# Kernel tuning notes

Measured on AMD Instinct MI355X. Metric: run time of the kernel, lower is better.

## Reference

```python
import jax, jax.numpy as jnp
import numpy as np

N = 100000   # nodes
E = 3200000  # edges (avg degree 32)
D = 128      # in_channels
H = 128      # hidden_channels
A, S, ETH = 3, 2, 3  # head output dims


def _w(k, o, i):
    return jax.random.normal(k, (o, i), dtype=jnp.float32) / np.sqrt(i).astype(np.float32)


def setup_inputs() -> dict:
    key = jax.random.key(0)
    ks = jax.random.split(key, 20)
    x = jax.random.normal(ks[0], (N, D), dtype=jnp.float32)
    edge_index = jax.random.randint(ks[1], (2, E), 0, N, dtype=jnp.int64)
    inp = {"x": x, "edge_index": edge_index}
    # SAGEConv params: Wl applied to mean-aggregated neighbors, Wr to root, plus bias
    dims = [("1", D, H), ("2", H, H), ("3", H, H), ("a", H, A), ("s", H, S), ("e", H, ETH)]
    ki = 2
    for tag, i, o in dims:
        inp[f"W{tag}l"] = _w(ks[ki], o, i); ki += 1
        inp[f"W{tag}r"] = _w(ks[ki], o, i); ki += 1
        inp[f"b{tag}"] = jnp.zeros((o,), dtype=jnp.float32)
    return inp


def _sage(x, src, dst, inv_deg, Wl, Wr, b):
    # mean aggregation of source features onto destination nodes, then linear
    agg = jax.ops.segment_sum(x[src], dst, num_segments=N) * inv_deg  # [N, d]
    return agg @ Wl.T + x @ Wr.T + b


def reference(x, edge_index,
              W1l, W1r, b1, W2l, W2r, b2, W3l, W3r, b3,
              Wal, War, ba, Wsl, Wsr, bs, Wel, Wer, be):
    src, dst = edge_index[0], edge_index[1]
    deg = jax.ops.segment_sum(jnp.ones((E,), jnp.float32), dst, num_segments=N)
    inv_deg = (1.0 / jnp.maximum(deg, 1.0))[:, None]  # [N,1]
    h = jax.nn.relu(_sage(x, src, dst, inv_deg, W1l, W1r, b1))
    h = jax.nn.relu(_sage(h, src, dst, inv_deg, W2l, W2r, b2))
    h = jax.nn.relu(_sage(h, src, dst, inv_deg, W3l, W3r, b3))
    age_out = _sage(h, src, dst, inv_deg, Wal, War, ba)
    sex_out = _sage(h, src, dst, inv_deg, Wsl, Wsr, bs)
    eth_out = _sage(h, src, dst, inv_deg, Wel, Wer, be)
    return (age_out, sex_out, eth_out)
```

## Files before the change

kernel.cpp:

```cpp
#include <hip/hip_runtime.h>

#define TPB 256
#define NB1 256
#define NBUCK 512

using half4_t = __attribute__((ext_vector_type(4))) _Float16;
using half8_t = __attribute__((ext_vector_type(8))) _Float16;
using f32x4 = __attribute__((ext_vector_type(4))) float;


__global__ __launch_bounds__(256) void hist1_k(const int* __restrict__ ei,
                                               int* __restrict__ hist, int E, int stripe) {
  __shared__ int h[NBUCK];
  for (int i = threadIdx.x; i < NBUCK; i += 256) h[i] = 0;
  __syncthreads();
  int b0 = blockIdx.x * stripe;
  int b1 = min(b0 + stripe, E);
  for (int e = b0 + threadIdx.x; e < b1; e += 256) atomicAdd(&h[ei[E + e] >> 8], 1);
  __syncthreads();
  for (int i = threadIdx.x; i < NBUCK; i += 256) hist[i * NB1 + blockIdx.x] = h[i];
}

__global__ void scan1_k(const int* __restrict__ src, int* __restrict__ out,
                        int* __restrict__ chunk, int n) {
  __shared__ int sh[TPB];
  int i = blockIdx.x * TPB + threadIdx.x;
  int v = (i < n) ? src[i] : 0;
  sh[threadIdx.x] = v;
  __syncthreads();
  for (int off = 1; off < TPB; off <<= 1) {
    int t = (threadIdx.x >= off) ? sh[threadIdx.x - off] : 0;
    __syncthreads();
    sh[threadIdx.x] += t;
    __syncthreads();
  }
  if (i < n) out[i] = sh[threadIdx.x] - v;
  if (threadIdx.x == TPB - 1) chunk[blockIdx.x] = sh[TPB - 1];
}

__global__ void scan2_k(int* __restrict__ chunk, int nb) {
  __shared__ int sh[512];
  int v = (threadIdx.x < nb) ? chunk[threadIdx.x] : 0;
  sh[threadIdx.x] = v;
  __syncthreads();
  for (int off = 1; off < 512; off <<= 1) {
    int t = (threadIdx.x >= off) ? sh[threadIdx.x - off] : 0;
    __syncthreads();
    sh[threadIdx.x] += t;
    __syncthreads();
  }
  if (threadIdx.x < nb) chunk[threadIdx.x] = sh[threadIdx.x] - v;
}

__global__ void scan3_k(int* __restrict__ out, const int* __restrict__ chunk, int n) {
  int i = blockIdx.x * TPB + threadIdx.x;
  if (i < n) out[i] += chunk[blockIdx.x];
}

__global__ __launch_bounds__(256) void scatter1_k(const int* __restrict__ ei,
                                                  const int* __restrict__ base,
                                                  unsigned* __restrict__ ebuf, int E,
                                                  int stripe) {
  __shared__ int cur[NBUCK];
  for (int i = threadIdx.x; i < NBUCK; i += 256) cur[i] = base[i * NB1 + blockIdx.x];
  __syncthreads();
  int b0 = blockIdx.x * stripe;
  int b1 = min(b0 + stripe, E);
  for (int e = b0 + threadIdx.x; e < b1; e += 256) {
    int s = ei[e];
    int d = ei[E + e];
    int p = atomicAdd(&cur[d >> 8], 1);
    ebuf[p] = (unsigned)s | ((unsigned)(d & 255) << 24);
  }
}

__global__ __launch_bounds__(256) void build_k(const unsigned* __restrict__ ebuf,
                                               const int* __restrict__ base,
                                               int* __restrict__ row_start,
                                               int* __restrict__ deg,
                                               float* __restrict__ invd,
                                               int* __restrict__ csr, int N, int E) {
  __shared__ int h[256];
  __shared__ int excl[256];
  __shared__ int bse[2];
  int b = blockIdx.x;
  int t = threadIdx.x;
  if (t == 0) {
    bse[0] = base[b * NB1];
    bse[1] = (b + 1 < NBUCK) ? base[(b + 1) * NB1] : E;
  }
  h[t] = 0;
  __syncthreads();
  int bs = bse[0], be = bse[1];
  for (int e = bs + t; e < be; e += 256) atomicAdd(&h[ebuf[e] >> 24], 1);
  __syncthreads();
  int v = h[t];
  excl[t] = v;
  __syncthreads();
  for (int off = 1; off < 256; off <<= 1) {
    int tv = (t >= off) ? excl[t - off] : 0;
    __syncthreads();
    excl[t] += tv;
    __syncthreads();
  }
  int ex = excl[t] - v;
  int node = b * 256 + t;
  if (node < N) {
    row_start[node] = bs + ex;
    deg[node] = v;
    invd[node] = 1.0f / fmaxf((float)v, 1.0f);
  }
  h[t] = bs + ex;
  __syncthreads();
  for (int e = bs + t; e < be; e += 256) {
    unsigned p = ebuf[e];
    int pos = atomicAdd(&h[p >> 24], 1);
    csr[pos] = (int)(p & 0xFFFFFFu);
  }
}


__global__ void prep_k(const float* __restrict__ x, _Float16* __restrict__ xh, int n4,
                       const float* __restrict__ w0, const float* __restrict__ w1,
                       const float* __restrict__ w2, const float* __restrict__ w3,
                       const float* __restrict__ w4, const float* __restrict__ w5,
                       _Float16* __restrict__ wh,
                       const float* __restrict__ Wal, const float* __restrict__ War,
                       const float* __restrict__ ba, const float* __restrict__ Wsl,
                       const float* __restrict__ Wsr, const float* __restrict__ bsx,
                       const float* __restrict__ Wel, const float* __restrict__ Wer,
                       const float* __restrict__ be, _Float16* __restrict__ Wcat,
                       float* __restrict__ bcat) {
  int t = blockIdx.x * TPB + threadIdx.x;
  if (t < n4) {
    float4 v = ((const float4*)x)[t];
    half4_t o;
    o.x = (_Float16)v.x; o.y = (_Float16)v.y; o.z = (_Float16)v.z; o.w = (_Float16)v.w;
    ((half4_t*)xh)[t] = o;
  }
  if (t < 6 * 4096) {
    int which = t >> 12, i = t & 4095;
    const float* src = which == 0 ? w0 : which == 1 ? w1 : which == 2 ? w2
                     : which == 3 ? w3 : which == 4 ? w4 : w5;
    float4 v = ((const float4*)src)[i];
    half4_t o;
    o.x = (_Float16)v.x; o.y = (_Float16)v.y; o.z = (_Float16)v.z; o.w = (_Float16)v.w;
    ((half4_t*)wh)[(size_t)which * 4096 + i] = o;
  }
  if (t < 2048) {
    float v = 0.f;
    if (t < 384) v = Wal[t];
    else if (t < 640) v = Wsl[t - 384];
    else if (t < 1024) v = Wel[t - 640];
    else if (t < 1408) v = War[t - 1024];
    else if (t < 1664) v = Wsr[t - 1408];
    else v = Wer[t - 1664];
    Wcat[t] = (_Float16)v;
  }
  if (t < 16) {
    float b = 0.f;
    if (t >= 8 && t < 11) b = ba[t - 8];
    else if (t >= 11 && t < 13) b = bsx[t - 11];
    else if (t >= 13) b = be[t - 13];
    bcat[t] = b;
  }
}


__global__ __launch_bounds__(256) void agg128_k(const _Float16* __restrict__ hb,
                                                const int* __restrict__ csr,
                                                const int* __restrict__ row_start,
                                                const int* __restrict__ deg,
                                                const float* __restrict__ invd,
                                                _Float16* __restrict__ out, int n) {
  int node = (blockIdx.x << 2) + (threadIdx.x >> 6);
  if (node >= n) return;
  int lane = threadIdx.x & 63;
  int g = lane >> 4;
  int l = lane & 15;
  int s = row_start[node];
  int c = deg[node];
  const _Float16* base = hb + (l << 3);
  float a0 = 0.f, a1 = 0.f, a2 = 0.f, a3 = 0.f;
  float a4 = 0.f, a5 = 0.f, a6 = 0.f, a7 = 0.f;
  int j = 0;
  if (c >= 16) {
    int id[4];
#pragma unroll
    for (int p = 0; p < 4; ++p) id[p] = csr[s + 4 * p + g];
    while (true) {
      half8_t v[4];
#pragma unroll
      for (int p = 0; p < 4; ++p) v[p] = *(const half8_t*)&base[(size_t)id[p] * 128];
      j += 16;
      bool more = (j + 16 <= c);
      if (more) {
#pragma unroll
        for (int p = 0; p < 4; ++p) id[p] = csr[s + j + 4 * p + g];
      }
#pragma unroll
      for (int p = 0; p < 4; ++p) {
        a0 += (float)v[p][0]; a1 += (float)v[p][1];
        a2 += (float)v[p][2]; a3 += (float)v[p][3];
        a4 += (float)v[p][4]; a5 += (float)v[p][5];
        a6 += (float)v[p][6]; a7 += (float)v[p][7];
      }
      if (!more) break;
    }
  }
  if (j < c) {
    int cm1 = c - 1;
#pragma unroll
    for (int p = 0; p < 4; ++p) {
      int e = j + 4 * p + g;
      float m = (e < c) ? 1.f : 0.f;
      int id = csr[s + min(e, cm1)];
      half8_t v = *(const half8_t*)&base[(size_t)id * 128];
      a0 = fmaf(m, (float)v[0], a0); a1 = fmaf(m, (float)v[1], a1);
      a2 = fmaf(m, (float)v[2], a2); a3 = fmaf(m, (float)v[3], a3);
      a4 = fmaf(m, (float)v[4], a4); a5 = fmaf(m, (float)v[5], a5);
      a6 = fmaf(m, (float)v[6], a6); a7 = fmaf(m, (float)v[7], a7);
    }
  }
  a0 += __shfl_xor(a0, 16); a1 += __shfl_xor(a1, 16);
  a2 += __shfl_xor(a2, 16); a3 += __shfl_xor(a3, 16);
  a4 += __shfl_xor(a4, 16); a5 += __shfl_xor(a5, 16);
  a6 += __shfl_xor(a6, 16); a7 += __shfl_xor(a7, 16);
  a0 += __shfl_xor(a0, 32); a1 += __shfl_xor(a1, 32);
  a2 += __shfl_xor(a2, 32); a3 += __shfl_xor(a3, 32);
  a4 += __shfl_xor(a4, 32); a5 += __shfl_xor(a5, 32);
  a6 += __shfl_xor(a6, 32); a7 += __shfl_xor(a7, 32);
  if (g == 0) {
    float w = invd[node];
    half8_t r;
    r[0] = (_Float16)(a0 * w); r[1] = (_Float16)(a1 * w);
    r[2] = (_Float16)(a2 * w); r[3] = (_Float16)(a3 * w);
    r[4] = (_Float16)(a4 * w); r[5] = (_Float16)(a5 * w);
    r[6] = (_Float16)(a6 * w); r[7] = (_Float16)(a7 * w);
    *(half8_t*)&out[(size_t)node * 128 + (l << 3)] = r;
  }
}


__global__ __launch_bounds__(256) void gemm2_k(
    const _Float16* __restrict__ Aagg, const _Float16* __restrict__ Ah,
    const _Float16* __restrict__ Wh,
    const float* __restrict__ bias, _Float16* __restrict__ outh, int n) {
  __shared__ _Float16 Ws[32768];
  int tid = threadIdx.x;
  int wave = tid >> 6;
  int lane = tid & 63;
  int g = lane >> 4;
  int l = lane & 15;
  int m0 = blockIdx.x * 64 + wave * 16;
  int arow = m0 + l;
  bool valid = arow < n;

  half8_t afA[4], afH[4];
  size_t abase = (size_t)arow * 128 + g * 8;
  if (valid) {
#pragma unroll
    for (int kb = 0; kb < 4; ++kb) afA[kb] = *(const half8_t*)&Aagg[abase + kb * 32];
#pragma unroll
    for (int kb = 0; kb < 4; ++kb) afH[kb] = *(const half8_t*)&Ah[abase + kb * 32];
  } else {
#pragma unroll
    for (int kb = 0; kb < 4; ++kb) {
#pragma unroll
      for (int jj = 0; jj < 8; ++jj) { afA[kb][jj] = (_Float16)0; afH[kb][jj] = (_Float16)0; }
    }
  }

#pragma unroll
  for (int it = 0; it < 16; ++it) {
    int ci = tid + it * 256;
    int row = ci >> 4;
    int kc = ci & 15;
    float4 v = *(const float4*)&Wh[(size_t)row * 128 + kc * 8];
    *(float4*)&Ws[(size_t)row * 128 + ((kc ^ (row & 7)) * 8)] = v;
  }
  __syncthreads();

  f32x4 acc[8];
#pragma unroll
  for (int ct = 0; ct < 8; ++ct) acc[ct] = (f32x4){0.f, 0.f, 0.f, 0.f};

#pragma unroll
  for (int kb = 0; kb < 4; ++kb) {
#pragma unroll
    for (int ct = 0; ct < 8; ++ct) {
      int row = ct * 16 + l;
      half8_t bf = *(const half8_t*)&Ws[(size_t)row * 128 + (((kb * 4 + g) ^ (l & 7)) * 8)];
      acc[ct] = __builtin_amdgcn_mfma_f32_16x16x32_f16(afA[kb], bf, acc[ct], 0, 0, 0);
    }
  }
#pragma unroll
  for (int kb = 0; kb < 4; ++kb) {
#pragma unroll
    for (int ct = 0; ct < 8; ++ct) {
      int row = 128 + ct * 16 + l;
      half8_t bf = *(const half8_t*)&Ws[(size_t)row * 128 + (((kb * 4 + g) ^ (l & 7)) * 8)];
      acc[ct] = __builtin_amdgcn_mfma_f32_16x16x32_f16(afH[kb], bf, acc[ct], 0, 0, 0);
    }
  }

#pragma unroll
  for (int ct = 0; ct < 8; ++ct) {
    int col = ct * 16 + l;
    float bc = bias[col];
#pragma unroll
    for (int r = 0; r < 4; ++r) {
      int row = m0 + g * 4 + r;
      if (row < n) {
        float v = fmaxf(acc[ct][r] + bc, 0.f);
        outh[(size_t)row * 128 + col] = (_Float16)v;
      }
    }
  }
}


__global__ __launch_bounds__(256) void head_gemm_k(const _Float16* __restrict__ h,
                                                   const _Float16* __restrict__ Wcat,
                                                   const float* __restrict__ bcat,
                                                   float* __restrict__ head_g,
                                                   float* __restrict__ head_r, int n) {
  __shared__ _Float16 Ws[2048];
  __shared__ float bs[16];
  int tid = threadIdx.x;
  {
    int row = tid >> 4, kc = tid & 15;
    float4 v = *(const float4*)&Wcat[(size_t)row * 128 + kc * 8];
    *(float4*)&Ws[(size_t)row * 128 + ((kc ^ (row & 7)) * 8)] = v;
    if (tid < 16) bs[tid] = bcat[tid];
  }
  __syncthreads();
  int wave = tid >> 6;
  int lane = tid & 63;
  int g = lane >> 4;
  int l = lane & 15;
  int m0 = blockIdx.x * 64 + wave * 16;
  int arow = m0 + l;
  bool valid = arow < n;
  size_t abase = (size_t)arow * 128 + g * 8;
  f32x4 acc = (f32x4){0.f, 0.f, 0.f, 0.f};
#pragma unroll
  for (int kb = 0; kb < 4; ++kb) {
    half8_t af;
    if (valid) {
      af = *(const half8_t*)&h[abase + kb * 32];
    } else {
#pragma unroll
      for (int jj = 0; jj < 8; ++jj) af[jj] = (_Float16)0;
    }
    half8_t bf = *(const half8_t*)&Ws[(size_t)l * 128 + (((kb * 4 + g) ^ (l & 7)) * 8)];
    acc = __builtin_amdgcn_mfma_f32_16x16x32_f16(af, bf, acc, 0, 0, 0);
  }
  float bc = bs[l];
#pragma unroll
  for (int r = 0; r < 4; ++r) {
    int row = m0 + g * 4 + r;
    if (row < n) {
      float v = acc[r] + bc;
      if (l < 8) head_g[(size_t)row * 8 + l] = v;
      else head_r[(size_t)row * 8 + (l - 8)] = v;
    }
  }
}


__global__ void agg8_k(const float* __restrict__ head_g, const float* __restrict__ head_r,
                       const int* __restrict__ csr, const int* __restrict__ row_start,
                       const int* __restrict__ deg, const float* __restrict__ invd,
                       float* __restrict__ out, int n) {
  int node = (blockIdx.x << 2) + (threadIdx.x >> 6);
  if (node >= n) return;
  int lane = threadIdx.x & 63;
  int c2 = lane & 3;
  int g = lane >> 2;
  int s = row_start[node], cnt = deg[node];
  float ax = 0.f, ay = 0.f;
  int j = 0;
  for (; j + 32 <= cnt; j += 32) {
#pragma unroll
    for (int p = 0; p < 2; ++p) {
      int id = csr[s + j + 16 * p + g];
      float2 v = *(const float2*)&head_g[(size_t)id * 8 + 2 * c2];
      ax += v.x;
      ay += v.y;
    }
  }
  if (j < cnt) {
    int cm1 = cnt - 1;
#pragma unroll
    for (int p = 0; p < 2; ++p) {
      int e = j + 16 * p + g;
      float m = (e < cnt) ? 1.f : 0.f;
      int id = csr[s + min(e, cm1)];
      float2 v = *(const float2*)&head_g[(size_t)id * 8 + 2 * c2];
      ax = fmaf(m, v.x, ax);
      ay = fmaf(m, v.y, ay);
    }
  }
  ax += __shfl_xor(ax, 4);  ay += __shfl_xor(ay, 4);
  ax += __shfl_xor(ax, 8);  ay += __shfl_xor(ay, 8);
  ax += __shfl_xor(ax, 16); ay += __shfl_xor(ay, 16);
  ax += __shfl_xor(ax, 32); ay += __shfl_xor(ay, 32);
  if (g == 0) {
    float w = invd[node];
    float r0 = ax * w + head_r[(size_t)node * 8 + 2 * c2];
    float r1 = ay * w + head_r[(size_t)node * 8 + 2 * c2 + 1];
    float rr[2] = {r0, r1};
#pragma unroll
    for (int q = 0; q < 2; ++q) {
      int f = 2 * c2 + q;
      float r = rr[q];
      if (f < 3) out[(size_t)node * 3 + f] = r;
      else if (f < 5) out[(size_t)3 * n + (size_t)node * 2 + (f - 3)] = r;
      else out[(size_t)5 * n + (size_t)node * 3 + (f - 5)] = r;
    }
  }
}


extern "C" void kernel_launch(void* const* d_in, const int* in_sizes, int n_in,
                              void* d_out, int out_size, void* d_ws, size_t ws_size,
                              hipStream_t stream) {
  const float* x = (const float*)d_in[0];
  const int* ei = (const int*)d_in[1];
  const float* W1l = (const float*)d_in[2];
  const float* W1r = (const float*)d_in[3];
  const float* b1 = (const float*)d_in[4];
  const float* W2l = (const float*)d_in[5];
  const float* W2r = (const float*)d_in[6];
  const float* b2 = (const float*)d_in[7];
  const float* W3l = (const float*)d_in[8];
  const float* W3r = (const float*)d_in[9];
  const float* b3 = (const float*)d_in[10];
  const float* Wal = (const float*)d_in[11];
  const float* War = (const float*)d_in[12];
  const float* ba = (const float*)d_in[13];
  const float* Wsl = (const float*)d_in[14];
  const float* Wsr = (const float*)d_in[15];
  const float* bsx = (const float*)d_in[16];
  const float* Wel = (const float*)d_in[17];
  const float* Wer = (const float*)d_in[18];
  const float* be = (const float*)d_in[19];

  int N = in_sizes[0] / 128;
  int E = in_sizes[1] / 2;
  int NBKT = (N + 255) >> 8;

  char* w = (char*)d_ws;
  auto alloc = [&](size_t b) {
    char* p = w;
    w += (b + 255) & ~(size_t)255;
    return p;
  };
  int* deg = (int*)alloc((size_t)N * 4);
  int* row_start = (int*)alloc((size_t)N * 4);
  float* invd = (float*)alloc((size_t)N * 4);
  int* hist = (int*)alloc((size_t)NBUCK * NB1 * 4);
  int* chunk = (int*)alloc(512 * 4);
  int* csr = (int*)alloc((size_t)E * 4);
  size_t xh_bytes = (size_t)N * 128 * 2;
  size_t ebuf_bytes = (size_t)E * 4;
  char* region = (char*)alloc(xh_bytes > ebuf_bytes ? xh_bytes : ebuf_bytes);
  unsigned* ebuf = (unsigned*)region;
  _Float16* xh = (_Float16*)region;
  _Float16* aggh = (_Float16*)alloc((size_t)N * 128 * 2);
  _Float16* hA = (_Float16*)alloc((size_t)N * 128 * 2);
  _Float16* hB = (_Float16*)alloc((size_t)N * 128 * 2);
  _Float16* wh = (_Float16*)alloc((size_t)6 * 16384 * 2);
  _Float16* Wcat = (_Float16*)alloc(2048 * 2);
  float* bcat = (float*)alloc(16 * 4);
  float* head_g = (float*)alloc((size_t)N * 8 * 4);
  float* head_r = (float*)alloc((size_t)N * 8 * 4);

  int stripe = (((E + NB1 - 1) / NB1) + 255) & ~255;
  int nscan = NBUCK * NB1;
  int nbScan = (nscan + TPB - 1) / TPB;
  int nbNode = (N + 3) / 4;
  int nbM = (N + 63) / 64;
  int nbC = (N * 32 + TPB - 1) / TPB;

  hist1_k<<<NB1, 256, 0, stream>>>(ei, hist, E, stripe);
  scan1_k<<<nbScan, TPB, 0, stream>>>(hist, hist, chunk, nscan);
  scan2_k<<<1, 512, 0, stream>>>(chunk, nbScan);
  scan3_k<<<nbScan, TPB, 0, stream>>>(hist, chunk, nscan);
  scatter1_k<<<NB1, 256, 0, stream>>>(ei, hist, ebuf, E, stripe);
  build_k<<<NBKT, 256, 0, stream>>>(ebuf, hist, row_start, deg, invd, csr, N, E);

  prep_k<<<nbC, TPB, 0, stream>>>(x, xh, N * 32, W1l, W1r, W2l, W2r, W3l, W3r, wh,
                                  Wal, War, ba, Wsl, Wsr, bsx, Wel, Wer, be, Wcat, bcat);

  agg128_k<<<nbNode, TPB, 0, stream>>>(xh, csr, row_start, deg, invd, aggh, N);
  gemm2_k<<<nbM, TPB, 0, stream>>>(aggh, xh, wh + 0 * 16384, b1, hA, N);
  agg128_k<<<nbNode, TPB, 0, stream>>>(hA, csr, row_start, deg, invd, aggh, N);
  gemm2_k<<<nbM, TPB, 0, stream>>>(aggh, hA, wh + 2 * 16384, b2, hB, N);
  agg128_k<<<nbNode, TPB, 0, stream>>>(hB, csr, row_start, deg, invd, aggh, N);
  gemm2_k<<<nbM, TPB, 0, stream>>>(aggh, hB, wh + 4 * 16384, b3, hA, N);
  head_gemm_k<<<nbM, TPB, 0, stream>>>(hA, Wcat, bcat, head_g, head_r, N);
  agg8_k<<<nbNode, TPB, 0, stream>>>(head_g, head_r, csr, row_start, deg, invd,
                                     (float*)d_out, N);
}
```

Measured before the change: 681.4 us.

## Split node features into four 32-channel planes and aggregate per plane

Feature tensors are stored as four planar 32-channel slabs instead of row-major 128 channels. Aggregation runs once per plane, so each gather touches a smaller working set (6.4 MB per plane) that is more likely to stay in cache. The aggregation also sums in fp16 vectors instead of fp32 scalars. That adds precision risk and four times as many aggregation launches and CSR index reads, and the GEMMs now read and write through plane-strided addresses.

Result: slower. 846.1 us (+24.2%).

```diff
diff --git a/kernel.cpp b/kernel.cpp
--- a/kernel.cpp
+++ b/kernel.cpp
@@ -120,7 +120,8 @@
 }
 
 
-__global__ void prep_k(const float* __restrict__ x, _Float16* __restrict__ xh, int n4,
+__global__ void prep_k(const float* __restrict__ x, _Float16* __restrict__ xhp, int n4,
+                       int N,
                        const float* __restrict__ w0, const float* __restrict__ w1,
                        const float* __restrict__ w2, const float* __restrict__ w3,
                        const float* __restrict__ w4, const float* __restrict__ w5,
@@ -136,7 +137,9 @@
     float4 v = ((const float4*)x)[t];
     half4_t o;
     o.x = (_Float16)v.x; o.y = (_Float16)v.y; o.z = (_Float16)v.z; o.w = (_Float16)v.w;
-    ((half4_t*)xh)[t] = o;
+    int node = t >> 5, w = t & 31;
+    int plane = w >> 3, off = (w & 7) * 4;
+    *(half4_t*)&xhp[(size_t)plane * N * 32 + (size_t)node * 32 + off] = o;
   }
   if (t < 6 * 4096) {
     int which = t >> 12, i = t & 4095;
@@ -167,77 +170,73 @@
 }
 
 
-__global__ __launch_bounds__(256) void agg128_k(const _Float16* __restrict__ hb,
-                                                const int* __restrict__ csr,
-                                                const int* __restrict__ row_start,
-                                                const int* __restrict__ deg,
-                                                const float* __restrict__ invd,
-                                                _Float16* __restrict__ out, int n) {
+static __device__ inline half8_t h8_shfl_xor(half8_t v, int m) {
+  union U { half8_t h; int i[4]; } u, r;
+  u.h = v;
+#pragma unroll
+  for (int k = 0; k < 4; ++k) r.i[k] = __shfl_xor(u.i[k], m);
+  return r.h;
+}
+
+__global__ __launch_bounds__(256) void agg32_k(const _Float16* __restrict__ hp,
+                                               const int* __restrict__ csr,
+                                               const int* __restrict__ row_start,
+                                               const int* __restrict__ deg,
+                                               const float* __restrict__ invd,
+                                               _Float16* __restrict__ outp, int n) {
   int node = (blockIdx.x << 2) + (threadIdx.x >> 6);
   if (node >= n) return;
   int lane = threadIdx.x & 63;
-  int g = lane >> 4;
-  int l = lane & 15;
+  int slot = lane >> 2;
+  int q = lane & 3;
   int s = row_start[node];
   int c = deg[node];
-  const _Float16* base = hb + (l << 3);
-  float a0 = 0.f, a1 = 0.f, a2 = 0.f, a3 = 0.f;
-  float a4 = 0.f, a5 = 0.f, a6 = 0.f, a7 = 0.f;
+  const _Float16* base = hp + (q << 3);
+  half8_t acc;
+#pragma unroll
+  for (int k = 0; k < 8; ++k) acc[k] = (_Float16)0;
   int j = 0;
-  if (c >= 16) {
-    int id[4];
-#pragma unroll
-    for (int p = 0; p < 4; ++p) id[p] = csr[s + 4 * p + g];
+  if (c >= 32) {
+    int idA = csr[s + slot];
+    int idB = csr[s + 16 + slot];
     while (true) {
-      half8_t v[4];
-#pragma unroll
-      for (int p = 0; p < 4; ++p) v[p] = *(const half8_t*)&base[(size_t)id[p] * 128];
-      j += 16;
-      bool more = (j + 16 <= c);
+      half8_t vA = *(const half8_t*)&base[(size_t)idA * 32];
+      half8_t vB = *(const half8_t*)&base[(size_t)idB * 32];
+      j += 32;
+      bool more = (j + 32 <= c);
       if (more) {
-#pragma unroll
-        for (int p = 0; p < 4; ++p) id[p] = csr[s + j + 4 * p + g];
+        idA = csr[s + j + slot];
+        idB = csr[s + j + 16 + slot];
       }
-#pragma unroll
-      for (int p = 0; p < 4; ++p) {
-        a0 += (float)v[p][0]; a1 += (float)v[p][1];
-        a2 += (float)v[p][2]; a3 += (float)v[p][3];
-        a4 += (float)v[p][4]; a5 += (float)v[p][5];
-        a6 += (float)v[p][6]; a7 += (float)v[p][7];
-      }
+      acc += vA;
+      acc += vB;
       if (!more) break;
     }
   }
   if (j < c) {
     int cm1 = c - 1;
 #pragma unroll
-    for (int p = 0; p < 4; ++p) {
-      int e = j + 4 * p + g;
-      float m = (e < c) ? 1.f : 0.f;
+    for (int p = 0; p < 2; ++p) {
+      int e = j + p * 16 + slot;
+      _Float16 m = (e < c) ? (_Float16)1 : (_Float16)0;
       int id = csr[s + min(e, cm1)];
-      half8_t v = *(const half8_t*)&base[(size_t)id * 128];
-      a0 = fmaf(m, (float)v[0], a0); a1 = fmaf(m, (float)v[1], a1);
-      a2 = fmaf(m, (float)v[2], a2); a3 = fmaf(m, (float)v[3], a3);
-      a4 = fmaf(m, (float)v[4], a4); a5 = fmaf(m, (float)v[5], a5);
-      a6 = fmaf(m, (float)v[6], a6); a7 = fmaf(m, (float)v[7], a7);
-    }
-  }
-  a0 += __shfl_xor(a0, 16); a1 += __shfl_xor(a1, 16);
-  a2 += __shfl_xor(a2, 16); a3 += __shfl_xor(a3, 16);
-  a4 += __shfl_xor(a4, 16); a5 += __shfl_xor(a5, 16);
-  a6 += __shfl_xor(a6, 16); a7 += __shfl_xor(a7, 16);
-  a0 += __shfl_xor(a0, 32); a1 += __shfl_xor(a1, 32);
-  a2 += __shfl_xor(a2, 32); a3 += __shfl_xor(a3, 32);
-  a4 += __shfl_xor(a4, 32); a5 += __shfl_xor(a5, 32);
-  a6 += __shfl_xor(a6, 32); a7 += __shfl_xor(a7, 32);
-  if (g == 0) {
+      half8_t v = *(const half8_t*)&base[(size_t)id * 32];
+      half8_t mm;
+#pragma unroll
+      for (int k = 0; k < 8; ++k) mm[k] = m;
+      acc += v * mm;
+    }
+  }
+  acc += h8_shfl_xor(acc, 4);
+  acc += h8_shfl_xor(acc, 8);
+  acc += h8_shfl_xor(acc, 16);
+  acc += h8_shfl_xor(acc, 32);
+  if (slot == 0) {
     float w = invd[node];
     half8_t r;
-    r[0] = (_Float16)(a0 * w); r[1] = (_Float16)(a1 * w);
-    r[2] = (_Float16)(a2 * w); r[3] = (_Float16)(a3 * w);
-    r[4] = (_Float16)(a4 * w); r[5] = (_Float16)(a5 * w);
-    r[6] = (_Float16)(a6 * w); r[7] = (_Float16)(a7 * w);
-    *(half8_t*)&out[(size_t)node * 128 + (l << 3)] = r;
+#pragma unroll
+    for (int k = 0; k < 8; ++k) r[k] = (_Float16)((float)acc[k] * w);
+    *(half8_t*)&outp[(size_t)node * 32 + (q << 3)] = r;
   }
 }
 
@@ -245,7 +244,7 @@
 __global__ __launch_bounds__(256) void gemm2_k(
     const _Float16* __restrict__ Aagg, const _Float16* __restrict__ Ah,
     const _Float16* __restrict__ Wh,
-    const float* __restrict__ bias, _Float16* __restrict__ outh, int n) {
+    const float* __restrict__ bias, _Float16* __restrict__ outh, int n, int N) {
   __shared__ _Float16 Ws[32768];
   int tid = threadIdx.x;
   int wave = tid >> 6;
@@ -255,14 +254,16 @@
   int m0 = blockIdx.x * 64 + wave * 16;
   int arow = m0 + l;
   bool valid = arow < n;
+  size_t pstride = (size_t)N * 32;
 
   half8_t afA[4], afH[4];
-  size_t abase = (size_t)arow * 128 + g * 8;
   if (valid) {
 #pragma unroll
-    for (int kb = 0; kb < 4; ++kb) afA[kb] = *(const half8_t*)&Aagg[abase + kb * 32];
-#pragma unroll
-    for (int kb = 0; kb < 4; ++kb) afH[kb] = *(const half8_t*)&Ah[abase + kb * 32];
+    for (int kb = 0; kb < 4; ++kb)
+      afA[kb] = *(const half8_t*)&Aagg[(size_t)kb * pstride + (size_t)arow * 32 + g * 8];
+#pragma unroll
+    for (int kb = 0; kb < 4; ++kb)
+      afH[kb] = *(const half8_t*)&Ah[(size_t)kb * pstride + (size_t)arow * 32 + g * 8];
   } else {
 #pragma unroll
     for (int kb = 0; kb < 4; ++kb) {
@@ -308,12 +309,13 @@
   for (int ct = 0; ct < 8; ++ct) {
     int col = ct * 16 + l;
     float bc = bias[col];
+    size_t pbase = (size_t)(ct >> 1) * pstride + (size_t)((ct & 1) * 16 + l);
 #pragma unroll
     for (int r = 0; r < 4; ++r) {
       int row = m0 + g * 4 + r;
       if (row < n) {
         float v = fmaxf(acc[ct][r] + bc, 0.f);
-        outh[(size_t)row * 128 + col] = (_Float16)v;
+        outh[pbase + (size_t)row * 32] = (_Float16)v;
       }
     }
   }
@@ -324,7 +326,8 @@
                                                    const _Float16* __restrict__ Wcat,
                                                    const float* __restrict__ bcat,
                                                    float* __restrict__ head_g,
-                                                   float* __restrict__ head_r, int n) {
+                                                   float* __restrict__ head_r, int n,
+                                                   int N) {
   __shared__ _Float16 Ws[2048];
   __shared__ float bs[16];
   int tid = threadIdx.x;
@@ -342,13 +345,13 @@
   int m0 = blockIdx.x * 64 + wave * 16;
   int arow = m0 + l;
   bool valid = arow < n;
-  size_t abase = (size_t)arow * 128 + g * 8;
+  size_t pstride = (size_t)N * 32;
   f32x4 acc = (f32x4){0.f, 0.f, 0.f, 0.f};
 #pragma unroll
   for (int kb = 0; kb < 4; ++kb) {
     half8_t af;
     if (valid) {
-      af = *(const half8_t*)&h[abase + kb * 32];
+      af = *(const half8_t*)&h[(size_t)kb * pstride + (size_t)arow * 32 + g * 8];
     } else {
 #pragma unroll
       for (int jj = 0; jj < 8; ++jj) af[jj] = (_Float16)0;
@@ -483,6 +486,7 @@
   int nbNode = (N + 3) / 4;
   int nbM = (N + 63) / 64;
   int nbC = (N * 32 + TPB - 1) / TPB;
+  size_t pstride = (size_t)N * 32;
 
   hist1_k<<<NB1, 256, 0, stream>>>(ei, hist, E, stripe);
   scan1_k<<<nbScan, TPB, 0, stream>>>(hist, hist, chunk, nscan);
@@ -491,16 +495,22 @@
   scatter1_k<<<NB1, 256, 0, stream>>>(ei, hist, ebuf, E, stripe);
   build_k<<<NBKT, 256, 0, stream>>>(ebuf, hist, row_start, deg, invd, csr, N, E);
 
-  prep_k<<<nbC, TPB, 0, stream>>>(x, xh, N * 32, W1l, W1r, W2l, W2r, W3l, W3r, wh,
+  prep_k<<<nbC, TPB, 0, stream>>>(x, xh, N * 32, N, W1l, W1r, W2l, W2r, W3l, W3r, wh,
                                   Wal, War, ba, Wsl, Wsr, bsx, Wel, Wer, be, Wcat, bcat);
 
-  agg128_k<<<nbNode, TPB, 0, stream>>>(xh, csr, row_start, deg, invd, aggh, N);
-  gemm2_k<<<nbM, TPB, 0, stream>>>(aggh, xh, wh + 0 * 16384, b1, hA, N);
-  agg128_k<<<nbNode, TPB, 0, stream>>>(hA, csr, row_start, deg, invd, aggh, N);
-  gemm2_k<<<nbM, TPB, 0, stream>>>(aggh, hA, wh + 2 * 16384, b2, hB, N);
-  agg128_k<<<nbNode, TPB, 0, stream>>>(hB, csr, row_start, deg, invd, aggh, N);
-  gemm2_k<<<nbM, TPB, 0, stream>>>(aggh, hB, wh + 4 * 16384, b3, hA, N);
-  head_gemm_k<<<nbM, TPB, 0, stream>>>(hA, Wcat, bcat, head_g, head_r, N);
+  for (int p = 0; p < 4; ++p)
+    agg32_k<<<nbNode, TPB, 0, stream>>>(xh + p * pstride, csr, row_start, deg, invd,
+                                        aggh + p * pstride, N);
+  gemm2_k<<<nbM, TPB, 0, stream>>>(aggh, xh, wh + 0 * 16384, b1, hA, N, N);
+  for (int p = 0; p < 4; ++p)
+    agg32_k<<<nbNode, TPB, 0, stream>>>(hA + p * pstride, csr, row_start, deg, invd,
+                                        aggh + p * pstride, N);
+  gemm2_k<<<nbM, TPB, 0, stream>>>(aggh, hA, wh + 2 * 16384, b2, hB, N, N);
+  for (int p = 0; p < 4; ++p)
+    agg32_k<<<nbNode, TPB, 0, stream>>>(hB + p * pstride, csr, row_start, deg, invd,
+                                        aggh + p * pstride, N);
+  gemm2_k<<<nbM, TPB, 0, stream>>>(aggh, hB, wh + 4 * 16384, b3, hA, N, N);
+  head_gemm_k<<<nbM, TPB, 0, stream>>>(hA, Wcat, bcat, head_g, head_r, N, N);
   agg8_k<<<nbNode, TPB, 0, stream>>>(head_g, head_r, csr, row_start, deg, invd,
                                      (float*)d_out, N);
 }
```

## Replace two-level bucketed CSR build with global-atomic degree count and fill

Applied to the files above, without the earlier changes.

Replaces the two-pass bucket sort (shared-memory histogram, scatter into bucketed buffer, per-bucket local sort) with a direct CSR build: global atomic degree count, scan over nodes, then a fill pass using global atomic cursors per destination. This removes the intermediate ebuf pass and the large histogram scan, but relies on millions of global atomics to random addresses and makes the neighbor order within each row nondeterministic. That order change can hurt gather locality in the aggregation kernels. Degree zeroing is folded into the prep kernel.

Result: slower. 972.4 us (+42.7%).

```diff
diff --git a/kernel.cpp b/kernel.cpp
--- a/kernel.cpp
+++ b/kernel.cpp
@@ -1,24 +1,15 @@
 #include <hip/hip_runtime.h>
 
 #define TPB 256
-#define NB1 256
-#define NBUCK 512
 
 using half4_t = __attribute__((ext_vector_type(4))) _Float16;
 using half8_t = __attribute__((ext_vector_type(8))) _Float16;
 using f32x4 = __attribute__((ext_vector_type(4))) float;
 
 
-__global__ __launch_bounds__(256) void hist1_k(const int* __restrict__ ei,
-                                               int* __restrict__ hist, int E, int stripe) {
-  __shared__ int h[NBUCK];
-  for (int i = threadIdx.x; i < NBUCK; i += 256) h[i] = 0;
-  __syncthreads();
-  int b0 = blockIdx.x * stripe;
-  int b1 = min(b0 + stripe, E);
-  for (int e = b0 + threadIdx.x; e < b1; e += 256) atomicAdd(&h[ei[E + e] >> 8], 1);
-  __syncthreads();
-  for (int i = threadIdx.x; i < NBUCK; i += 256) hist[i * NB1 + blockIdx.x] = h[i];
+__global__ void deg_k(const int* __restrict__ ei, int* __restrict__ deg, int E) {
+  int e = blockIdx.x * TPB + threadIdx.x;
+  if (e < E) atomicAdd(&deg[ei[E + e]], 1);
 }
 
 __global__ void scan1_k(const int* __restrict__ src, int* __restrict__ out,
@@ -52,75 +43,32 @@
   if (threadIdx.x < nb) chunk[threadIdx.x] = sh[threadIdx.x] - v;
 }
 
-__global__ void scan3_k(int* __restrict__ out, const int* __restrict__ chunk, int n) {
+__global__ void scan3b_k(int* __restrict__ row_start, const int* __restrict__ chunk,
+                         int* __restrict__ cursor, const int* __restrict__ deg,
+                         float* __restrict__ invd, int n) {
   int i = blockIdx.x * TPB + threadIdx.x;
-  if (i < n) out[i] += chunk[blockIdx.x];
-}
-
-__global__ __launch_bounds__(256) void scatter1_k(const int* __restrict__ ei,
-                                                  const int* __restrict__ base,
-                                                  unsigned* __restrict__ ebuf, int E,
-                                                  int stripe) {
-  __shared__ int cur[NBUCK];
-  for (int i = threadIdx.x; i < NBUCK; i += 256) cur[i] = base[i * NB1 + blockIdx.x];
-  __syncthreads();
-  int b0 = blockIdx.x * stripe;
-  int b1 = min(b0 + stripe, E);
-  for (int e = b0 + threadIdx.x; e < b1; e += 256) {
+  if (i < n) {
+    int rs = row_start[i] + chunk[blockIdx.x];
+    row_start[i] = rs;
+    cursor[i] = rs;
+    invd[i] = 1.0f / fmaxf((float)deg[i], 1.0f);
+  }
+}
+
+__global__ void fill_k(const int* __restrict__ ei, int* __restrict__ cursor,
+                       int* __restrict__ csr, int E) {
+  int e = blockIdx.x * TPB + threadIdx.x;
+  if (e < E) {
     int s = ei[e];
     int d = ei[E + e];
-    int p = atomicAdd(&cur[d >> 8], 1);
-    ebuf[p] = (unsigned)s | ((unsigned)(d & 255) << 24);
-  }
-}
-
-__global__ __launch_bounds__(256) void build_k(const unsigned* __restrict__ ebuf,
-                                               const int* __restrict__ base,
-                                               int* __restrict__ row_start,
-                                               int* __restrict__ deg,
-                                               float* __restrict__ invd,
-                                               int* __restrict__ csr, int N, int E) {
-  __shared__ int h[256];
-  __shared__ int excl[256];
-  __shared__ int bse[2];
-  int b = blockIdx.x;
-  int t = threadIdx.x;
-  if (t == 0) {
-    bse[0] = base[b * NB1];
-    bse[1] = (b + 1 < NBUCK) ? base[(b + 1) * NB1] : E;
-  }
-  h[t] = 0;
-  __syncthreads();
-  int bs = bse[0], be = bse[1];
-  for (int e = bs + t; e < be; e += 256) atomicAdd(&h[ebuf[e] >> 24], 1);
-  __syncthreads();
-  int v = h[t];
-  excl[t] = v;
-  __syncthreads();
-  for (int off = 1; off < 256; off <<= 1) {
-    int tv = (t >= off) ? excl[t - off] : 0;
-    __syncthreads();
-    excl[t] += tv;
-    __syncthreads();
-  }
-  int ex = excl[t] - v;
-  int node = b * 256 + t;
-  if (node < N) {
-    row_start[node] = bs + ex;
-    deg[node] = v;
-    invd[node] = 1.0f / fmaxf((float)v, 1.0f);
-  }
-  h[t] = bs + ex;
-  __syncthreads();
-  for (int e = bs + t; e < be; e += 256) {
-    unsigned p = ebuf[e];
-    int pos = atomicAdd(&h[p >> 24], 1);
-    csr[pos] = (int)(p & 0xFFFFFFu);
+    int pos = atomicAdd(&cursor[d], 1);
+    csr[pos] = s;
   }
 }
 
 
 __global__ void prep_k(const float* __restrict__ x, _Float16* __restrict__ xh, int n4,
+                       int* __restrict__ deg, int N,
                        const float* __restrict__ w0, const float* __restrict__ w1,
                        const float* __restrict__ w2, const float* __restrict__ w3,
                        const float* __restrict__ w4, const float* __restrict__ w5,
@@ -138,6 +86,7 @@
     o.x = (_Float16)v.x; o.y = (_Float16)v.y; o.z = (_Float16)v.z; o.w = (_Float16)v.w;
     ((half4_t*)xh)[t] = o;
   }
+  if (t < N) deg[t] = 0;
   if (t < 6 * 4096) {
     int which = t >> 12, i = t & 4095;
     const float* src = which == 0 ? w0 : which == 1 ? w1 : which == 2 ? w2
@@ -449,7 +398,6 @@
 
   int N = in_sizes[0] / 128;
   int E = in_sizes[1] / 2;
-  int NBKT = (N + 255) >> 8;
 
   char* w = (char*)d_ws;
   auto alloc = [&](size_t b) {
@@ -459,15 +407,11 @@
   };
   int* deg = (int*)alloc((size_t)N * 4);
   int* row_start = (int*)alloc((size_t)N * 4);
+  int* cursor = (int*)alloc((size_t)N * 4);
   float* invd = (float*)alloc((size_t)N * 4);
-  int* hist = (int*)alloc((size_t)NBUCK * NB1 * 4);
   int* chunk = (int*)alloc(512 * 4);
   int* csr = (int*)alloc((size_t)E * 4);
-  size_t xh_bytes = (size_t)N * 128 * 2;
-  size_t ebuf_bytes = (size_t)E * 4;
-  char* region = (char*)alloc(xh_bytes > ebuf_bytes ? xh_bytes : ebuf_bytes);
-  unsigned* ebuf = (unsigned*)region;
-  _Float16* xh = (_Float16*)region;
+  _Float16* xh = (_Float16*)alloc((size_t)N * 128 * 2);
   _Float16* aggh = (_Float16*)alloc((size_t)N * 128 * 2);
   _Float16* hA = (_Float16*)alloc((size_t)N * 128 * 2);
   _Float16* hB = (_Float16*)alloc((size_t)N * 128 * 2);
@@ -477,22 +421,20 @@
   float* head_g = (float*)alloc((size_t)N * 8 * 4);
   float* head_r = (float*)alloc((size_t)N * 8 * 4);
 
-  int stripe = (((E + NB1 - 1) / NB1) + 255) & ~255;
-  int nscan = NBUCK * NB1;
-  int nbScan = (nscan + TPB - 1) / TPB;
   int nbNode = (N + 3) / 4;
   int nbM = (N + 63) / 64;
   int nbC = (N * 32 + TPB - 1) / TPB;
-
-  hist1_k<<<NB1, 256, 0, stream>>>(ei, hist, E, stripe);
-  scan1_k<<<nbScan, TPB, 0, stream>>>(hist, hist, chunk, nscan);
+  int nbE = (E + TPB - 1) / TPB;
+  int nbScan = (N + TPB - 1) / TPB;
+
+  prep_k<<<nbC, TPB, 0, stream>>>(x, xh, N * 32, deg, N, W1l, W1r, W2l, W2r, W3l, W3r,
+                                  wh, Wal, War, ba, Wsl, Wsr, bsx, Wel, Wer, be, Wcat,
+                                  bcat);
+  deg_k<<<nbE, TPB, 0, stream>>>(ei, deg, E);
+  scan1_k<<<nbScan, TPB, 0, stream>>>(deg, row_start, chunk, N);
   scan2_k<<<1, 512, 0, stream>>>(chunk, nbScan);
-  scan3_k<<<nbScan, TPB, 0, stream>>>(hist, chunk, nscan);
-  scatter1_k<<<NB1, 256, 0, stream>>>(ei, hist, ebuf, E, stripe);
-  build_k<<<NBKT, 256, 0, stream>>>(ebuf, hist, row_start, deg, invd, csr, N, E);
-
-  prep_k<<<nbC, TPB, 0, stream>>>(x, xh, N * 32, W1l, W1r, W2l, W2r, W3l, W3r, wh,
-                                  Wal, War, ba, Wsl, Wsr, bsx, Wel, Wer, be, Wcat, bcat);
+  scan3b_k<<<nbScan, TPB, 0, stream>>>(row_start, chunk, cursor, deg, invd, N);
+  fill_k<<<nbE, TPB, 0, stream>>>(ei, cursor, csr, E);
 
   agg128_k<<<nbNode, TPB, 0, stream>>>(xh, csr, row_start, deg, invd, aggh, N);
   gemm2_k<<<nbM, TPB, 0, stream>>>(aggh, xh, wh + 0 * 16384, b1, hA, N);
```

## Fuse histogram with prep, fold scan fixup into consumers, fuse head GEMM

Applied to the files above, without the earlier changes.

Merges the edge histogram and the input/weight fp16 conversion into one launch, which needs separate ebuf and xh buffers instead of an aliased region. Drops the scan3 pass by adding the per-chunk offsets directly in scatter and build. Fuses the head projection into the last layer GEMM epilogue: the ReLU output goes to shared memory and is multiplied by the concatenated head weights, so the layer-3 hidden state is never written to or reread from global memory. This saves launches and a full N×128 round trip, at the cost of extra workspace and a heavier GEMM epilogue.

Measured after the change: 656.2 us. 3.7% less time.

```diff
diff --git a/kernel.cpp b/kernel.cpp
--- a/kernel.cpp
+++ b/kernel.cpp
@@ -9,16 +9,64 @@
 using f32x4 = __attribute__((ext_vector_type(4))) float;
 
 
-__global__ __launch_bounds__(256) void hist1_k(const int* __restrict__ ei,
-                                               int* __restrict__ hist, int E, int stripe) {
+__global__ __launch_bounds__(256) void histprep_k(
+    const int* __restrict__ ei, int* __restrict__ hist, int E, int stripe,
+    const float* __restrict__ x, _Float16* __restrict__ xh, int n4,
+    const float* __restrict__ w0, const float* __restrict__ w1,
+    const float* __restrict__ w2, const float* __restrict__ w3,
+    const float* __restrict__ w4, const float* __restrict__ w5,
+    _Float16* __restrict__ wh,
+    const float* __restrict__ Wal, const float* __restrict__ War,
+    const float* __restrict__ ba, const float* __restrict__ Wsl,
+    const float* __restrict__ Wsr, const float* __restrict__ bsx,
+    const float* __restrict__ Wel, const float* __restrict__ Wer,
+    const float* __restrict__ be, _Float16* __restrict__ Wcat,
+    float* __restrict__ bcat) {
   __shared__ int h[NBUCK];
-  for (int i = threadIdx.x; i < NBUCK; i += 256) h[i] = 0;
-  __syncthreads();
-  int b0 = blockIdx.x * stripe;
-  int b1 = min(b0 + stripe, E);
-  for (int e = b0 + threadIdx.x; e < b1; e += 256) atomicAdd(&h[ei[E + e] >> 8], 1);
-  __syncthreads();
-  for (int i = threadIdx.x; i < NBUCK; i += 256) hist[i * NB1 + blockIdx.x] = h[i];
+  int b = blockIdx.x;
+  if (b < NB1) {
+    for (int i = threadIdx.x; i < NBUCK; i += 256) h[i] = 0;
+    __syncthreads();
+    int b0 = b * stripe;
+    int b1 = min(b0 + stripe, E);
+    for (int e = b0 + threadIdx.x; e < b1; e += 256) atomicAdd(&h[ei[E + e] >> 8], 1);
+    __syncthreads();
+    for (int i = threadIdx.x; i < NBUCK; i += 256) hist[i * NB1 + b] = h[i];
+    return;
+  }
+  int t = (b - NB1) * TPB + threadIdx.x;
+  if (t < n4) {
+    float4 v = ((const float4*)x)[t];
+    half4_t o;
+    o.x = (_Float16)v.x; o.y = (_Float16)v.y; o.z = (_Float16)v.z; o.w = (_Float16)v.w;
+    ((half4_t*)xh)[t] = o;
+  }
+  if (t < 6 * 4096) {
+    int which = t >> 12, i = t & 4095;
+    const float* src = which == 0 ? w0 : which == 1 ? w1 : which == 2 ? w2
+                     : which == 3 ? w3 : which == 4 ? w4 : w5;
+    float4 v = ((const float4*)src)[i];
+    half4_t o;
+    o.x = (_Float16)v.x; o.y = (_Float16)v.y; o.z = (_Float16)v.z; o.w = (_Float16)v.w;
+    ((half4_t*)wh)[(size_t)which * 4096 + i] = o;
+  }
+  if (t < 2048) {
+    float v = 0.f;
+    if (t < 384) v = Wal[t];
+    else if (t < 640) v = Wsl[t - 384];
+    else if (t < 1024) v = Wel[t - 640];
+    else if (t < 1408) v = War[t - 1024];
+    else if (t < 1664) v = Wsr[t - 1408];
+    else v = Wer[t - 1664];
+    Wcat[t] = (_Float16)v;
+  }
+  if (t < 16) {
+    float bb = 0.f;
+    if (t >= 8 && t < 11) bb = ba[t - 8];
+    else if (t >= 11 && t < 13) bb = bsx[t - 11];
+    else if (t >= 13) bb = be[t - 13];
+    bcat[t] = bb;
+  }
 }
 
 __global__ void scan1_k(const int* __restrict__ src, int* __restrict__ out,
@@ -52,17 +100,15 @@
   if (threadIdx.x < nb) chunk[threadIdx.x] = sh[threadIdx.x] - v;
 }
 
-__global__ void scan3_k(int* __restrict__ out, const int* __restrict__ chunk, int n) {
-  int i = blockIdx.x * TPB + threadIdx.x;
-  if (i < n) out[i] += chunk[blockIdx.x];
-}
 
 __global__ __launch_bounds__(256) void scatter1_k(const int* __restrict__ ei,
                                                   const int* __restrict__ base,
+                                                  const int* __restrict__ chunk,
                                                   unsigned* __restrict__ ebuf, int E,
                                                   int stripe) {
   __shared__ int cur[NBUCK];
-  for (int i = threadIdx.x; i < NBUCK; i += 256) cur[i] = base[i * NB1 + blockIdx.x];
+  for (int i = threadIdx.x; i < NBUCK; i += 256)
+    cur[i] = base[i * NB1 + blockIdx.x] + chunk[i];
   __syncthreads();
   int b0 = blockIdx.x * stripe;
   int b1 = min(b0 + stripe, E);
@@ -76,6 +122,7 @@
 
 __global__ __launch_bounds__(256) void build_k(const unsigned* __restrict__ ebuf,
                                                const int* __restrict__ base,
+                                               const int* __restrict__ chunk,
                                                int* __restrict__ row_start,
                                                int* __restrict__ deg,
                                                float* __restrict__ invd,
@@ -86,8 +133,8 @@
   int b = blockIdx.x;
   int t = threadIdx.x;
   if (t == 0) {
-    bse[0] = base[b * NB1];
-    bse[1] = (b + 1 < NBUCK) ? base[(b + 1) * NB1] : E;
+    bse[0] = base[b * NB1] + chunk[b];
+    bse[1] = (b + 1 < NBUCK) ? base[(b + 1) * NB1] + chunk[b + 1] : E;
   }
   h[t] = 0;
   __syncthreads();
@@ -116,53 +163,6 @@
     unsigned p = ebuf[e];
     int pos = atomicAdd(&h[p >> 24], 1);
     csr[pos] = (int)(p & 0xFFFFFFu);
-  }
-}
-
-
-__global__ void prep_k(const float* __restrict__ x, _Float16* __restrict__ xh, int n4,
-                       const float* __restrict__ w0, const float* __restrict__ w1,
-                       const float* __restrict__ w2, const float* __restrict__ w3,
-                       const float* __restrict__ w4, const float* __restrict__ w5,
-                       _Float16* __restrict__ wh,
-                       const float* __restrict__ Wal, const float* __restrict__ War,
-                       const float* __restrict__ ba, const float* __restrict__ Wsl,
-                       const float* __restrict__ Wsr, const float* __restrict__ bsx,
-                       const float* __restrict__ Wel, const float* __restrict__ Wer,
-                       const float* __restrict__ be, _Float16* __restrict__ Wcat,
-                       float* __restrict__ bcat) {
-  int t = blockIdx.x * TPB + threadIdx.x;
-  if (t < n4) {
-    float4 v = ((const float4*)x)[t];
-    half4_t o;
-    o.x = (_Float16)v.x; o.y = (_Float16)v.y; o.z = (_Float16)v.z; o.w = (_Float16)v.w;
-    ((half4_t*)xh)[t] = o;
-  }
-  if (t < 6 * 4096) {
-    int which = t >> 12, i = t & 4095;
-    const float* src = which == 0 ? w0 : which == 1 ? w1 : which == 2 ? w2
-                     : which == 3 ? w3 : which == 4 ? w4 : w5;
-    float4 v = ((const float4*)src)[i];
-    half4_t o;
-    o.x = (_Float16)v.x; o.y = (_Float16)v.y; o.z = (_Float16)v.z; o.w = (_Float16)v.w;
-    ((half4_t*)wh)[(size_t)which * 4096 + i] = o;
-  }
-  if (t < 2048) {
-    float v = 0.f;
-    if (t < 384) v = Wal[t];
-    else if (t < 640) v = Wsl[t - 384];
-    else if (t < 1024) v = Wel[t - 640];
-    else if (t < 1408) v = War[t - 1024];
-    else if (t < 1664) v = Wsr[t - 1408];
-    else v = Wer[t - 1664];
-    Wcat[t] = (_Float16)v;
-  }
-  if (t < 16) {
-    float b = 0.f;
-    if (t >= 8 && t < 11) b = ba[t - 8];
-    else if (t >= 11 && t < 13) b = bsx[t - 11];
-    else if (t >= 13) b = be[t - 13];
-    bcat[t] = b;
   }
 }
 
@@ -245,7 +245,9 @@
 __global__ __launch_bounds__(256) void gemm2_k(
     const _Float16* __restrict__ Aagg, const _Float16* __restrict__ Ah,
     const _Float16* __restrict__ Wh,
-    const float* __restrict__ bias, _Float16* __restrict__ outh, int n) {
+    const float* __restrict__ bias, _Float16* __restrict__ outh,
+    const _Float16* __restrict__ Wcat, const float* __restrict__ bcat,
+    float* __restrict__ head_g, float* __restrict__ head_r, int n, int mode) {
   __shared__ _Float16 Ws[32768];
   int tid = threadIdx.x;
   int wave = tid >> 6;
@@ -304,66 +306,48 @@
     }
   }
 
-#pragma unroll
-  for (int ct = 0; ct < 8; ++ct) {
-    int col = ct * 16 + l;
-    float bc = bias[col];
+  if (mode == 0) {
+#pragma unroll
+    for (int ct = 0; ct < 8; ++ct) {
+      int col = ct * 16 + l;
+      float bc = bias[col];
+#pragma unroll
+      for (int r = 0; r < 4; ++r) {
+        int row = m0 + g * 4 + r;
+        if (row < n) {
+          float v = fmaxf(acc[ct][r] + bc, 0.f);
+          outh[(size_t)row * 128 + col] = (_Float16)v;
+        }
+      }
+    }
+  } else {
+    __syncthreads();
+    _Float16* Hs = Ws + wave * 2048;
+#pragma unroll
+    for (int ct = 0; ct < 8; ++ct) {
+      int col = ct * 16 + l;
+      float bc = bias[col];
+#pragma unroll
+      for (int r = 0; r < 4; ++r) {
+        Hs[(g * 4 + r) * 128 + col] = (_Float16)fmaxf(acc[ct][r] + bc, 0.f);
+      }
+    }
+    f32x4 ah = (f32x4){0.f, 0.f, 0.f, 0.f};
+#pragma unroll
+    for (int kb = 0; kb < 4; ++kb) {
+      half8_t af = *(const half8_t*)&Hs[l * 128 + kb * 32 + g * 8];
+      half8_t bf = *(const half8_t*)&Wcat[(size_t)l * 128 + kb * 32 + g * 8];
+      ah = __builtin_amdgcn_mfma_f32_16x16x32_f16(af, bf, ah, 0, 0, 0);
+    }
+    float bc = bcat[l];
 #pragma unroll
     for (int r = 0; r < 4; ++r) {
       int row = m0 + g * 4 + r;
       if (row < n) {
-        float v = fmaxf(acc[ct][r] + bc, 0.f);
-        outh[(size_t)row * 128 + col] = (_Float16)v;
+        float v = ah[r] + bc;
+        if (l < 8) head_g[(size_t)row * 8 + l] = v;
+        else head_r[(size_t)row * 8 + (l - 8)] = v;
       }
-    }
-  }
-}
-
-
-__global__ __launch_bounds__(256) void head_gemm_k(const _Float16* __restrict__ h,
-                                                   const _Float16* __restrict__ Wcat,
-                                                   const float* __restrict__ bcat,
-                                                   float* __restrict__ head_g,
-                                                   float* __restrict__ head_r, int n) {
-  __shared__ _Float16 Ws[2048];
-  __shared__ float bs[16];
-  int tid = threadIdx.x;
-  {
-    int row = tid >> 4, kc = tid & 15;
-    float4 v = *(const float4*)&Wcat[(size_t)row * 128 + kc * 8];
-    *(float4*)&Ws[(size_t)row * 128 + ((kc ^ (row & 7)) * 8)] = v;
-    if (tid < 16) bs[tid] = bcat[tid];
-  }
-  __syncthreads();
-  int wave = tid >> 6;
-  int lane = tid & 63;
-  int g = lane >> 4;
-  int l = lane & 15;
-  int m0 = blockIdx.x * 64 + wave * 16;
-  int arow = m0 + l;
-  bool valid = arow < n;
-  size_t abase = (size_t)arow * 128 + g * 8;
-  f32x4 acc = (f32x4){0.f, 0.f, 0.f, 0.f};
-#pragma unroll
-  for (int kb = 0; kb < 4; ++kb) {
-    half8_t af;
-    if (valid) {
-      af = *(const half8_t*)&h[abase + kb * 32];
-    } else {
-#pragma unroll
-      for (int jj = 0; jj < 8; ++jj) af[jj] = (_Float16)0;
-    }
-    half8_t bf = *(const half8_t*)&Ws[(size_t)l * 128 + (((kb * 4 + g) ^ (l & 7)) * 8)];
-    acc = __builtin_amdgcn_mfma_f32_16x16x32_f16(af, bf, acc, 0, 0, 0);
-  }
-  float bc = bs[l];
-#pragma unroll
-  for (int r = 0; r < 4; ++r) {
-    int row = m0 + g * 4 + r;
-    if (row < n) {
-      float v = acc[r] + bc;
-      if (l < 8) head_g[(size_t)row * 8 + l] = v;
-      else head_r[(size_t)row * 8 + (l - 8)] = v;
     }
   }
 }
@@ -463,11 +447,8 @@
   int* hist = (int*)alloc((size_t)NBUCK * NB1 * 4);
   int* chunk = (int*)alloc(512 * 4);
   int* csr = (int*)alloc((size_t)E * 4);
-  size_t xh_bytes = (size_t)N * 128 * 2;
-  size_t ebuf_bytes = (size_t)E * 4;
-  char* region = (char*)alloc(xh_bytes > ebuf_bytes ? xh_bytes : ebuf_bytes);
-  unsigned* ebuf = (unsigned*)region;
-  _Float16* xh = (_Float16*)region;
+  unsigned* ebuf = (unsigned*)alloc((size_t)E * 4);
+  _Float16* xh = (_Float16*)alloc((size_t)N * 128 * 2);
   _Float16* aggh = (_Float16*)alloc((size_t)N * 128 * 2);
   _Float16* hA = (_Float16*)alloc((size_t)N * 128 * 2);
   _Float16* hB = (_Float16*)alloc((size_t)N * 128 * 2);
@@ -484,23 +465,24 @@
   int nbM = (N + 63) / 64;
   int nbC = (N * 32 + TPB - 1) / TPB;
 
-  hist1_k<<<NB1, 256, 0, stream>>>(ei, hist, E, stripe);
+  histprep_k<<<NB1 + nbC, TPB, 0, stream>>>(ei, hist, E, stripe, x, xh, N * 32,
+                                            W1l, W1r, W2l, W2r, W3l, W3r, wh,
+                                            Wal, War, ba, Wsl, Wsr, bsx, Wel, Wer,
+                                            be, Wcat, bcat);
   scan1_k<<<nbScan, TPB, 0, stream>>>(hist, hist, chunk, nscan);
   scan2_k<<<1, 512, 0, stream>>>(chunk, nbScan);
-  scan3_k<<<nbScan, TPB, 0, stream>>>(hist, chunk, nscan);
-  scatter1_k<<<NB1, 256, 0, stream>>>(ei, hist, ebuf, E, stripe);
-  build_k<<<NBKT, 256, 0, stream>>>(ebuf, hist, row_start, deg, invd, csr, N, E);
-
-  prep_k<<<nbC, TPB, 0, stream>>>(x, xh, N * 32, W1l, W1r, W2l, W2r, W3l, W3r, wh,
-                                  Wal, War, ba, Wsl, Wsr, bsx, Wel, Wer, be, Wcat, bcat);
+  scatter1_k<<<NB1, 256, 0, stream>>>(ei, hist, chunk, ebuf, E, stripe);
+  build_k<<<NBKT, 256, 0, stream>>>(ebuf, hist, chunk, row_start, deg, invd, csr, N, E);
 
   agg128_k<<<nbNode, TPB, 0, stream>>>(xh, csr, row_start, deg, invd, aggh, N);
-  gemm2_k<<<nbM, TPB, 0, stream>>>(aggh, xh, wh + 0 * 16384, b1, hA, N);
+  gemm2_k<<<nbM, TPB, 0, stream>>>(aggh, xh, wh + 0 * 16384, b1, hA, nullptr, nullptr,
+                                   nullptr, nullptr, N, 0);
   agg128_k<<<nbNode, TPB, 0, stream>>>(hA, csr, row_start, deg, invd, aggh, N);
-  gemm2_k<<<nbM, TPB, 0, stream>>>(aggh, hA, wh + 2 * 16384, b2, hB, N);
+  gemm2_k<<<nbM, TPB, 0, stream>>>(aggh, hA, wh + 2 * 16384, b2, hB, nullptr, nullptr,
+                                   nullptr, nullptr, N, 0);
   agg128_k<<<nbNode, TPB, 0, stream>>>(hB, csr, row_start, deg, invd, aggh, N);
-  gemm2_k<<<nbM, TPB, 0, stream>>>(aggh, hB, wh + 4 * 16384, b3, hA, N);
-  head_gemm_k<<<nbM, TPB, 0, stream>>>(hA, Wcat, bcat, head_g, head_r, N);
+  gemm2_k<<<nbM, TPB, 0, stream>>>(aggh, hB, wh + 4 * 16384, b3, nullptr, Wcat, bcat,
+                                   head_g, head_r, N, 1);
   agg8_k<<<nbNode, TPB, 0, stream>>>(head_g, head_r, csr, row_start, deg, invd,
                                      (float*)d_out, N);
 }
```
